# Kernel optimization log

Measured on AMD Instinct MI355X. Metric: run time of the kernel, lower is better.

Reference implementation:

```python
import jax, jax.numpy as jnp
import numpy as np

T, B, DG, DH, S = 24, 128, 256, 512, 3
LAM, ETA, EPS_A = 0.95, 0.5, 1e-6   # lambda_decay, eta, epsilon (A-update)
LN_EPS = 1e-5                        # torch LayerNorm default eps
EPS_N = 1e-6                         # norm clamp in inner loop


def setup_inputs() -> dict:
    key = jax.random.key(0)
    ks = jax.random.split(key, 3)
    return {
        "z_seq": jax.random.normal(ks[0], (T, B, DG), jnp.float32),
        "W_h": jax.random.normal(ks[1], (DH, DH), jnp.float32) * (2.0 / DH) ** 0.5,  # kaiming-ish
        "W_g": jax.random.normal(ks[2], (DH, DG), jnp.float32) * (1.0 / DG) ** 0.5,  # xavier-ish
        "b_h": jnp.zeros((DH,), jnp.float32),
        "gamma": jnp.ones((DH,), jnp.float32),
        "beta": jnp.zeros((DH,), jnp.float32),
        "alpha_fw": jnp.ones((1,), jnp.float32),
    }


def _layernorm(x, g, b):
    m = jnp.mean(x, -1, keepdims=True)
    v = jnp.mean((x - m) ** 2, -1, keepdims=True)
    return (x - m) * jax.lax.rsqrt(v + LN_EPS) * g + b


def _compute_k(a):
    k_pos = 1.0 + jax.nn.softplus(a)
    k_neg = 1.0 / (1.0 + jax.nn.softplus(-a))
    return jnp.where(a >= 0, k_pos, k_neg)


def reference(z_seq, W_h, W_g, b_h, gamma, beta, alpha_fw):
    k = _compute_k(alpha_fw[0])

    def step(carry, inp):
        h, A = carry            # h: [B, DH], A: [B, DH, DH]
        z_t, upd = inp          # z_t: [B, DG], upd: scalar bool (t < T-1)
        h_base = h @ W_h.T + z_t @ W_g.T + b_h
        h_s = jax.nn.relu(h_base)
        for _ in range(S):      # inner associative-memory iteration
            Ah = jnp.einsum('bij,bj->bi', A, h_s)
            dot = jnp.sum(h_s * Ah, -1, keepdims=True)
            n1 = jnp.maximum(jnp.linalg.norm(h_s, axis=-1, keepdims=True), EPS_N)
            n2 = jnp.maximum(jnp.linalg.norm(Ah, axis=-1, keepdims=True), EPS_N)
            R_pos = jnp.clip(dot / (n1 * n2), 0.0, 1.0)
            alpha_dyn = 1.0 - (1.0 - R_pos) ** k
            h_s = jax.nn.relu(_layernorm((1.0 - alpha_dyn ** 2) * h_base + alpha_dyn * Ah, gamma, beta))
        # fast-weight Hebbian update (skipped at the last timestep)
        hn2 = jnp.sum(h_s ** 2, -1, keepdims=True) + EPS_A            # [B, 1]
        delta = h_s[:, :, None] * h_s[:, None, :] / hn2[:, :, None]   # [B, DH, DH]
        A_new = jnp.where(upd, LAM * A + ETA * delta, A)
        return (h_s, A_new), None

    h0 = jnp.zeros((B, DH), z_seq.dtype)
    A0 = jnp.zeros((B, DH, DH), z_seq.dtype)
    upd = jnp.arange(T) < (T - 1)
    (h, A), _ = jax.lax.scan(step, (h0, A0), (z_seq, upd))
    return h
```

## Files before the change

kernel.cpp:

```cpp
#include <hip/hip_runtime.h>
#include <hip/hip_fp16.h>
#include <math.h>

#define T_STEPS 24
#define BATCH   128
#define DGI     256
#define DHI     512
#define S_ITERS 3
#define LAMBDA  0.95f
#define ETA     0.5f
#define EPS_A   1e-6f
#define LN_EPS  1e-5f
#define EPS_N   1e-6f
#define HIST_MAX 23

static __device__ __forceinline__ float dot2(unsigned int a, unsigned int b, float c) {
#if __has_builtin(__builtin_amdgcn_fdot2)
    typedef _Float16 h2v __attribute__((ext_vector_type(2)));
    return __builtin_amdgcn_fdot2(__builtin_bit_cast(h2v, a),
                                  __builtin_bit_cast(h2v, b), c, false);
#else
    const __half2 ha = __builtin_bit_cast(__half2, a);
    const __half2 hb = __builtin_bit_cast(__half2, b);
    const float2 fa = __half22float2(ha);
    const float2 fb = __half22float2(hb);
    return fmaf(fa.x, fb.x, fmaf(fa.y, fb.y, c));
#endif
}

__global__ __launch_bounds__(512)
void pack_wh_k(const float* __restrict__ Wh, unsigned int* __restrict__ P) {
    const int j2 = blockIdx.x;
    const int i  = threadIdx.x;
    const float2 w = *(const float2*)(Wh + (size_t)i * DHI + 2 * j2);
    const __half2 h = __floats2half2_rn(w.x, w.y);
    P[(size_t)j2 * DHI + i] = __builtin_bit_cast(unsigned int, h);
}

__global__ __launch_bounds__(512)
void zproj_k(const float* __restrict__ z_seq, const float* __restrict__ Wg,
             float* __restrict__ zp) {
    __shared__ __align__(16) float sh_z[8][DGI];
    const int b    = blockIdx.x;
    const int t0   = blockIdx.y * 8;
    const int tid  = threadIdx.x;
    const int lane = tid & 63;
    const int wave = tid >> 6;
    {
        const float4* src =
            (const float4*)(z_seq + ((size_t)(t0 + wave) * BATCH + b) * DGI);
        ((float4*)sh_z[wave])[lane] = src[lane];
    }
    __syncthreads();

    float acc[8];
    #pragma unroll
    for (int tt = 0; tt < 8; ++tt) acc[tt] = 0.f;
    const float4* wrow = (const float4*)(Wg + (size_t)tid * DGI);
    #pragma unroll 4
    for (int j4 = 0; j4 < DGI / 4; ++j4) {
        const float4 w = wrow[j4];
        #pragma unroll
        for (int tt = 0; tt < 8; ++tt) {
            const float4 z = ((const float4*)sh_z[tt])[j4];
            acc[tt] = fmaf(w.x, z.x, acc[tt]);
            acc[tt] = fmaf(w.y, z.y, acc[tt]);
            acc[tt] = fmaf(w.z, z.z, acc[tt]);
            acc[tt] = fmaf(w.w, z.w, acc[tt]);
        }
    }
    #pragma unroll
    for (int tt = 0; tt < 8; ++tt)
        zp[((size_t)b * T_STEPS + (t0 + tt)) * DHI + tid] = acc[tt];
}

__global__ __launch_bounds__(512)
void rnn_fp16w(const float* __restrict__ zp,
               const unsigned int* __restrict__ P,
               const float* __restrict__ b_h,
               const float* __restrict__ gamma,
               const float* __restrict__ beta,
               const float* __restrict__ alpha_fw,
               float* __restrict__ out) {
    __shared__ __align__(16) float  sh_hist[HIST_MAX][DHI];
    __shared__ __align__(16) float  sh_hs[2][DHI];
    __shared__ __align__(16) float  sh_G[HIST_MAX][64];
    __shared__ __align__(16) float4 sh_part[4][128];
    __shared__ __align__(16) unsigned int sh_h2[DHI / 2];
    __shared__ float  sh_coef[32];
    __shared__ float  sh_dot[32];
    __shared__ float2 sh_red[8];

    const int tid  = threadIdx.x;
    const int lane = tid & 63;
    const int wave = tid >> 6;
    const int b    = blockIdx.x;

    const float bh_r = b_h[tid];
    const float g_r  = gamma[tid];
    const float bt_r = beta[tid];

    float kpow;
    {
        const float a  = alpha_fw[0];
        const float ax = fabsf(a);
        const float sp = (ax > 20.f) ? ax : log1pf(expf(ax));
        kpow = (a >= 0.f) ? (1.f + sp) : (1.f / (1.f + sp));
    }

    for (int i = tid; i < HIST_MAX * 64; i += DHI) ((float*)sh_G)[i] = 0.f;
    __syncthreads();

    int   p = 0;
    float hs_i = 0.f, hbase_i = 0.f;

    for (int t = 0; t < T_STEPS; ++t) {
        const float zval = zp[((size_t)b * T_STEPS + t) * DHI + tid];
        if (t > 0) {
            const int i4 = tid & 127;
            const int jg = tid >> 7;
            const uint4* __restrict__ wp = (const uint4*)P;
            float4 acc = make_float4(0.f, 0.f, 0.f, 0.f);
            const int j2lo = jg * 64;
            #pragma unroll 8
            for (int jj = 0; jj < 64; ++jj) {
                const int j2 = j2lo + jj;
                const unsigned int hh = sh_h2[j2];
                const uint4 wv = wp[(size_t)j2 * 128 + i4];
                acc.x = dot2(wv.x, hh, acc.x);
                acc.y = dot2(wv.y, hh, acc.y);
                acc.z = dot2(wv.z, hh, acc.z);
                acc.w = dot2(wv.w, hh, acc.w);
            }
            sh_part[jg][i4] = acc;
            __syncthreads();
            const float* pp = (const float*)sh_part;
            hbase_i = bh_r + zval +
                      ((pp[tid] + pp[512 + tid]) + (pp[1024 + tid] + pp[1536 + tid]));
        } else {
            hbase_i = bh_r + zval;
        }
        hs_i = fmaxf(hbase_i, 0.f);
        p ^= 1;
        sh_hs[p][tid] = hs_i;
        __syncthreads();

        const int niter = (t == 0) ? 1 : S_ITERS;
        for (int it = 0; it < niter; ++it) {
            const float* hcur = sh_hs[p];
            float h8[8];
            #pragma unroll
            for (int q = 0; q < 8; ++q) h8[q] = hcur[lane + 64 * q];

            for (int s = wave; s <= t; s += 8) {
                float d = 0.f;
                if (s == t) {
                    #pragma unroll
                    for (int q = 0; q < 8; ++q) d = fmaf(h8[q], h8[q], d);
                } else {
                    const float* vr = sh_hist[s];
                    #pragma unroll
                    for (int q = 0; q < 8; ++q) d = fmaf(vr[lane + 64 * q], h8[q], d);
                }
                #pragma unroll
                for (int off = 32; off > 0; off >>= 1) d += __shfl_xor(d, off, 64);
                if (lane == 0) sh_dot[s] = d;
            }
            __syncthreads();

            float dl = 0.f, w_l = 0.f;
            if (lane < t) { dl = sh_dot[lane]; w_l = sh_coef[lane] * dl; }

            float gsum = 0.f, Ah = 0.f;
            for (int s = 0; s < t; ++s) {
                const float ws = sh_coef[s] * sh_dot[s];
                gsum = fmaf(ws, sh_G[s][lane], gsum);
                Ah   = fmaf(ws, sh_hist[s][tid], Ah);
            }
            float pa = w_l * dl;
            float pb = w_l * gsum;
            #pragma unroll
            for (int off = 32; off > 0; off >>= 1) {
                pa += __shfl_xor(pa, off, 64);
                pb += __shfl_xor(pb, off, 64);
            }
            const float n1 = fmaxf(sqrtf(sh_dot[t]), EPS_N);
            const float n2 = fmaxf(sqrtf(fmaxf(pb, 0.f)), EPS_N);
            float R = pa / (n1 * n2);
            R = fminf(fmaxf(R, 0.f), 1.f);
            const float alpha = 1.f - __powf(1.f - R, kpow);

            const float y = (1.f - alpha * alpha) * hbase_i + alpha * Ah;

            float q0 = y, q1 = y * y;
            #pragma unroll
            for (int off = 32; off > 0; off >>= 1) {
                q0 += __shfl_xor(q0, off, 64);
                q1 += __shfl_xor(q1, off, 64);
            }
            if (lane == 0) sh_red[wave] = make_float2(q0, q1);
            __syncthreads();

            float s0 = 0.f, s1 = 0.f;
            #pragma unroll
            for (int w = 0; w < 8; ++w) {
                const float2 r = sh_red[w];
                s0 += r.x; s1 += r.y;
            }
            const float mean = s0 * (1.f / DHI);
            const float var  = fmaf(s1, 1.f / DHI, -mean * mean);
            const float rstd = rsqrtf(var + LN_EPS);
            hs_i = fmaxf(fmaf((y - mean) * rstd, g_r, bt_r), 0.f);
            p ^= 1;
            sh_hs[p][tid] = hs_i;
            if (it == niter - 1 && t + 1 < T_STEPS) {
                const float partner = __shfl_xor(hs_i, 1);
                if (!(tid & 1)) {
                    const __half2 h2 = __floats2half2_rn(hs_i, partner);
                    sh_h2[tid >> 1] = __builtin_bit_cast(unsigned int, h2);
                }
            }
            __syncthreads();
        }

        if (t < T_STEPS - 1) {
            const float* hcur = sh_hs[p];
            float h8[8];
            #pragma unroll
            for (int q = 0; q < 8; ++q) h8[q] = hcur[lane + 64 * q];
            for (int s = wave; s <= t; s += 8) {
                float d = 0.f;
                if (s == t) {
                    #pragma unroll
                    for (int q = 0; q < 8; ++q) d = fmaf(h8[q], h8[q], d);
                } else {
                    const float* vr = sh_hist[s];
                    #pragma unroll
                    for (int q = 0; q < 8; ++q) d = fmaf(vr[lane + 64 * q], h8[q], d);
                }
                #pragma unroll
                for (int off = 32; off > 0; off >>= 1) d += __shfl_xor(d, off, 64);
                if (lane == 0) {
                    if (s == t) {
                        sh_G[t][t] = d;
                        sh_coef[t] = ETA / (d + EPS_A);
                    } else {
                        sh_G[t][s] = d;
                        sh_G[s][t] = d;
                    }
                }
            }
            if (tid < t) sh_coef[tid] *= LAMBDA;
            sh_hist[t][tid] = hs_i;
        } else {
            out[(size_t)b * DHI + tid] = hs_i;
        }
    }
}

__global__ __launch_bounds__(512)
void corernn_fb(const float* __restrict__ z_seq, const float* __restrict__ Wh,
                const float* __restrict__ Wg, const float* __restrict__ b_h,
                const float* __restrict__ gamma, const float* __restrict__ beta,
                const float* __restrict__ alpha_fw, float* __restrict__ out) {
    __shared__ __align__(16) float sh_hist[HIST_MAX][DHI];
    __shared__ __align__(16) float sh_hs[2][DHI];
    __shared__ __align__(16) float sh_G[HIST_MAX][64];
    __shared__ float  sh_coef[32];
    __shared__ float  sh_dot[32];
    __shared__ float2 sh_red[8];
    __shared__ __align__(16) float sh_z[DGI];

    const int tid  = threadIdx.x;
    const int lane = tid & 63;
    const int wave = tid >> 6;
    const int b    = blockIdx.x;
    const float bh_r = b_h[tid];
    const float g_r  = gamma[tid];
    const float bt_r = beta[tid];
    float kpow;
    {
        const float a  = alpha_fw[0];
        const float ax = fabsf(a);
        const float sp = (ax > 20.f) ? ax : log1pf(expf(ax));
        kpow = (a >= 0.f) ? (1.f + sp) : (1.f / (1.f + sp));
    }
    for (int i = tid; i < HIST_MAX * 64; i += DHI) ((float*)sh_G)[i] = 0.f;
    if (tid < DGI) sh_z[tid] = z_seq[(size_t)b * DGI + tid];
    __syncthreads();

    int p = 0;
    float hs_i = 0.f, hbase_i = 0.f;
    for (int t = 0; t < T_STEPS; ++t) {
        float a0 = bh_r, a1 = 0.f, a2 = 0.f, a3 = 0.f;
        {
            const float4* wrow = (const float4*)(Wg + (size_t)tid * DGI);
            const float4* z4   = (const float4*)sh_z;
            #pragma unroll 4
            for (int j4 = 0; j4 < DGI / 4; ++j4) {
                const float4 w = wrow[j4]; const float4 h = z4[j4];
                a0 = fmaf(w.x, h.x, a0); a1 = fmaf(w.y, h.y, a1);
                a2 = fmaf(w.z, h.z, a2); a3 = fmaf(w.w, h.w, a3);
            }
        }
        if (t > 0) {
            const float4* wrow = (const float4*)(Wh + (size_t)tid * DHI);
            const float4* h4   = (const float4*)sh_hs[p];
            #pragma unroll 4
            for (int j4 = 0; j4 < DHI / 4; ++j4) {
                const float4 w = wrow[j4]; const float4 h = h4[j4];
                a0 = fmaf(w.x, h.x, a0); a1 = fmaf(w.y, h.y, a1);
                a2 = fmaf(w.z, h.z, a2); a3 = fmaf(w.w, h.w, a3);
            }
        }
        hbase_i = (a0 + a1) + (a2 + a3);
        hs_i = fmaxf(hbase_i, 0.f);
        p ^= 1; sh_hs[p][tid] = hs_i;
        __syncthreads();

        const int niter = (t == 0) ? 1 : S_ITERS;
        for (int it = 0; it < niter; ++it) {
            const float* hcur = sh_hs[p];
            float h8[8];
            #pragma unroll
            for (int q = 0; q < 8; ++q) h8[q] = hcur[lane + 64 * q];
            for (int s = wave; s <= t; s += 8) {
                float d = 0.f;
                if (s == t) {
                    #pragma unroll
                    for (int q = 0; q < 8; ++q) d = fmaf(h8[q], h8[q], d);
                } else {
                    const float* vr = sh_hist[s];
                    #pragma unroll
                    for (int q = 0; q < 8; ++q) d = fmaf(vr[lane + 64 * q], h8[q], d);
                }
                #pragma unroll
                for (int off = 32; off > 0; off >>= 1) d += __shfl_xor(d, off, 64);
                if (lane == 0) sh_dot[s] = d;
            }
            __syncthreads();
            float dl = 0.f, w_l = 0.f;
            if (lane < t) { dl = sh_dot[lane]; w_l = sh_coef[lane] * dl; }
            float gsum = 0.f, Ah = 0.f;
            for (int s = 0; s < t; ++s) {
                const float ws = sh_coef[s] * sh_dot[s];
                gsum = fmaf(ws, sh_G[s][lane], gsum);
                Ah   = fmaf(ws, sh_hist[s][tid], Ah);
            }
            float pa = w_l * dl, pb = w_l * gsum;
            #pragma unroll
            for (int off = 32; off > 0; off >>= 1) {
                pa += __shfl_xor(pa, off, 64);
                pb += __shfl_xor(pb, off, 64);
            }
            const float n1 = fmaxf(sqrtf(sh_dot[t]), EPS_N);
            const float n2 = fmaxf(sqrtf(fmaxf(pb, 0.f)), EPS_N);
            float R = fminf(fmaxf(pa / (n1 * n2), 0.f), 1.f);
            const float alpha = 1.f - __powf(1.f - R, kpow);
            const float y = (1.f - alpha * alpha) * hbase_i + alpha * Ah;
            float q0 = y, q1 = y * y;
            #pragma unroll
            for (int off = 32; off > 0; off >>= 1) {
                q0 += __shfl_xor(q0, off, 64);
                q1 += __shfl_xor(q1, off, 64);
            }
            if (lane == 0) sh_red[wave] = make_float2(q0, q1);
            __syncthreads();
            float s0 = 0.f, s1 = 0.f;
            #pragma unroll
            for (int w = 0; w < 8; ++w) { const float2 r = sh_red[w]; s0 += r.x; s1 += r.y; }
            const float mean = s0 * (1.f / DHI);
            const float var  = fmaf(s1, 1.f / DHI, -mean * mean);
            const float rstd = rsqrtf(var + LN_EPS);
            hs_i = fmaxf(fmaf((y - mean) * rstd, g_r, bt_r), 0.f);
            p ^= 1; sh_hs[p][tid] = hs_i;
            if (it == niter - 1 && t + 1 < T_STEPS && tid < DGI)
                sh_z[tid] = z_seq[((size_t)(t + 1) * BATCH + b) * DGI + tid];
            __syncthreads();
        }

        if (t < T_STEPS - 1) {
            const float* hcur = sh_hs[p];
            float h8[8];
            #pragma unroll
            for (int q = 0; q < 8; ++q) h8[q] = hcur[lane + 64 * q];
            for (int s = wave; s <= t; s += 8) {
                float d = 0.f;
                if (s == t) {
                    #pragma unroll
                    for (int q = 0; q < 8; ++q) d = fmaf(h8[q], h8[q], d);
                } else {
                    const float* vr = sh_hist[s];
                    #pragma unroll
                    for (int q = 0; q < 8; ++q) d = fmaf(vr[lane + 64 * q], h8[q], d);
                }
                #pragma unroll
                for (int off = 32; off > 0; off >>= 1) d += __shfl_xor(d, off, 64);
                if (lane == 0) {
                    if (s == t) { sh_G[t][t] = d; sh_coef[t] = ETA / (d + EPS_A); }
                    else        { sh_G[t][s] = d; sh_G[s][t] = d; }
                }
            }
            if (tid < t) sh_coef[tid] *= LAMBDA;
            sh_hist[t][tid] = hs_i;
        } else {
            out[(size_t)b * DHI + tid] = hs_i;
        }
    }
}

extern "C" void kernel_launch(void* const* d_in, const int* in_sizes, int n_in,
                              void* d_out, int out_size, void* d_ws, size_t ws_size,
                              hipStream_t stream) {
    const float* z_seq    = (const float*)d_in[0];
    const float* W_h      = (const float*)d_in[1];
    const float* W_g      = (const float*)d_in[2];
    const float* b_h      = (const float*)d_in[3];
    const float* gamma    = (const float*)d_in[4];
    const float* beta     = (const float*)d_in[5];
    const float* alpha_fw = (const float*)d_in[6];
    float* out = (float*)d_out;

    const size_t zp_elems = (size_t)BATCH * T_STEPS * DHI;
    const size_t p_elems  = (size_t)(DHI / 2) * DHI;
    const size_t needed   = zp_elems * sizeof(float) + p_elems * sizeof(unsigned int);
    if (ws_size >= needed) {
        float* zp = (float*)d_ws;
        unsigned int* P = (unsigned int*)(zp + zp_elems);
        pack_wh_k<<<DHI / 2, DHI, 0, stream>>>(W_h, P);
        zproj_k<<<dim3(BATCH, T_STEPS / 8), 512, 0, stream>>>(z_seq, W_g, zp);
        rnn_fp16w<<<BATCH, DHI, 0, stream>>>(zp, P, b_h, gamma, beta, alpha_fw, out);
    } else {
        corernn_fb<<<BATCH, DHI, 0, stream>>>(z_seq, W_h, W_g, b_h, gamma, beta,
                                              alpha_fw, out);
    }
}
```

Before: 409.3 us.

## Compute LayerNorm stats algebraically and restructure history reductions and projections

The LayerNorm mean and variance inside the inner loop are now derived from precomputed scalar sums over the history (row sums, dots with h_base, the Gram-weighted norm), which removes a block-wide reduction and barrier per iteration. The history is also kept in a transposed float4 layout so each thread accumulates Ah and the Gram terms four steps at a time. Hidden-state halves are broadcast with readlane instead of LDS reads, and the next step's z projection is prefetched early. The z projection now uses a transposed W_g with readlane broadcasts, which needs an extra transpose kernel and more workspace. The algebraic variance can lose precision through cancellation, so it is clamped at zero.

```diff
diff --git a/kernel.cpp b/kernel.cpp
--- a/kernel.cpp
+++ b/kernel.cpp
@@ -13,6 +13,7 @@
 #define LN_EPS  1e-5f
 #define EPS_N   1e-6f
 #define HIST_MAX 23
+#define NG4      6
 
 static __device__ __forceinline__ float dot2(unsigned int a, unsigned int b, float c) {
 #if __has_builtin(__builtin_amdgcn_fdot2)
@@ -28,6 +29,49 @@
 #endif
 }
 
+static __device__ __forceinline__ unsigned int rdlane_u(unsigned int v, int l) {
+#if __has_builtin(__builtin_amdgcn_readlane)
+    return __builtin_amdgcn_readlane(v, l);
+#else
+    return __shfl((int)v, l, 64);
+#endif
+}
+static __device__ __forceinline__ float rdlane_f(float v, int l) {
+    return __uint_as_float(rdlane_u(__float_as_uint(v), l));
+}
+
+static __device__ __forceinline__ float wsum(float v) {
+    #pragma unroll
+    for (int off = 32; off > 0; off >>= 1) v += __shfl_xor(v, off, 64);
+    return v;
+}
+static __device__ __forceinline__ float dot8(float4 a, float4 b, float4 c, float4 d) {
+    float r = a.x * c.x;
+    r = fmaf(a.y, c.y, r); r = fmaf(a.z, c.z, r); r = fmaf(a.w, c.w, r);
+    r = fmaf(b.x, d.x, r); r = fmaf(b.y, d.y, r); r = fmaf(b.z, d.z, r);
+    r = fmaf(b.w, d.w, r);
+    return r;
+}
+static __device__ __forceinline__ float sum8(float4 a, float4 b) {
+    return ((a.x + a.y) + (a.z + a.w)) + ((b.x + b.y) + (b.z + b.w));
+}
+
+__global__ void transpose_k(const float* __restrict__ src, float* __restrict__ dst,
+                            int R, int C) {
+    __shared__ float tile[32][33];
+    const int tx = threadIdx.x & 31;
+    const int ty = threadIdx.x >> 5;
+    const int c0 = blockIdx.x * 32;
+    const int r0 = blockIdx.y * 32;
+    #pragma unroll
+    for (int i = 0; i < 32; i += 8)
+        tile[ty + i][tx] = src[(size_t)(r0 + ty + i) * C + (c0 + tx)];
+    __syncthreads();
+    #pragma unroll
+    for (int i = 0; i < 32; i += 8)
+        dst[(size_t)(c0 + ty + i) * R + (r0 + tx)] = tile[tx][ty + i];
+}
+
 __global__ __launch_bounds__(512)
 void pack_wh_k(const float* __restrict__ Wh, unsigned int* __restrict__ P) {
     const int j2 = blockIdx.x;
@@ -38,9 +82,10 @@
 }
 
 __global__ __launch_bounds__(512)
-void zproj_k(const float* __restrict__ z_seq, const float* __restrict__ Wg,
+void zproj_k(const float* __restrict__ z_seq, const float* __restrict__ WgT,
              float* __restrict__ zp) {
-    __shared__ __align__(16) float sh_z[8][DGI];
+    __shared__ __align__(16) float  sh_z[8][DGI];
+    __shared__ __align__(16) float4 sh_acc[8][4][128];
     const int b    = blockIdx.x;
     const int t0   = blockIdx.y * 8;
     const int tid  = threadIdx.x;
@@ -53,43 +98,64 @@
     }
     __syncthreads();
 
-    float acc[8];
-    #pragma unroll
-    for (int tt = 0; tt < 8; ++tt) acc[tt] = 0.f;
-    const float4* wrow = (const float4*)(Wg + (size_t)tid * DGI);
+    const int i4  = tid & 127;
+    const int jg  = tid >> 7;
+    const int jlo = jg * 64;
+    float zreg[8];
+    #pragma unroll
+    for (int tt = 0; tt < 8; ++tt) zreg[tt] = sh_z[tt][jlo + lane];
+
+    float4 acc[8];
+    #pragma unroll
+    for (int tt = 0; tt < 8; ++tt) acc[tt] = make_float4(0.f, 0.f, 0.f, 0.f);
+
+    const float4* w4 = (const float4*)WgT;
     #pragma unroll 4
-    for (int j4 = 0; j4 < DGI / 4; ++j4) {
-        const float4 w = wrow[j4];
+    for (int jj = 0; jj < 64; ++jj) {
+        const float4 wv = w4[(size_t)(jlo + jj) * 128 + i4];
         #pragma unroll
         for (int tt = 0; tt < 8; ++tt) {
-            const float4 z = ((const float4*)sh_z[tt])[j4];
-            acc[tt] = fmaf(w.x, z.x, acc[tt]);
-            acc[tt] = fmaf(w.y, z.y, acc[tt]);
-            acc[tt] = fmaf(w.z, z.z, acc[tt]);
-            acc[tt] = fmaf(w.w, z.w, acc[tt]);
-        }
-    }
-    #pragma unroll
-    for (int tt = 0; tt < 8; ++tt)
-        zp[((size_t)b * T_STEPS + (t0 + tt)) * DHI + tid] = acc[tt];
+            const float zv = rdlane_f(zreg[tt], jj);
+            acc[tt].x = fmaf(wv.x, zv, acc[tt].x);
+            acc[tt].y = fmaf(wv.y, zv, acc[tt].y);
+            acc[tt].z = fmaf(wv.z, zv, acc[tt].z);
+            acc[tt].w = fmaf(wv.w, zv, acc[tt].w);
+        }
+    }
+    #pragma unroll
+    for (int tt = 0; tt < 8; ++tt) sh_acc[tt][jg][i4] = acc[tt];
+    __syncthreads();
+
+    const float* af = (const float*)sh_acc;
+    #pragma unroll
+    for (int tt = 0; tt < 8; ++tt) {
+        const int o = tt * 4 * 512;
+        const float v = (af[o + tid] + af[o + 512 + tid]) +
+                        (af[o + 1024 + tid] + af[o + 1536 + tid]);
+        zp[((size_t)b * T_STEPS + t0 + tt) * DHI + tid] = v;
+    }
 }
 
 __global__ __launch_bounds__(512)
-void rnn_fp16w(const float* __restrict__ zp,
-               const unsigned int* __restrict__ P,
-               const float* __restrict__ b_h,
-               const float* __restrict__ gamma,
-               const float* __restrict__ beta,
-               const float* __restrict__ alpha_fw,
-               float* __restrict__ out) {
+void rnn_v3(const float* __restrict__ zp,
+            const unsigned int* __restrict__ P,
+            const float* __restrict__ b_h,
+            const float* __restrict__ gamma,
+            const float* __restrict__ beta,
+            const float* __restrict__ alpha_fw,
+            float* __restrict__ out) {
     __shared__ __align__(16) float  sh_hist[HIST_MAX][DHI];
+    __shared__ __align__(16) float4 sh_hT4[NG4][DHI];
+    __shared__ __align__(16) float4 sh_G4[NG4][64];
     __shared__ __align__(16) float  sh_hs[2][DHI];
-    __shared__ __align__(16) float  sh_G[HIST_MAX][64];
+    __shared__ __align__(16) float  sh_hb[DHI];
     __shared__ __align__(16) float4 sh_part[4][128];
     __shared__ __align__(16) unsigned int sh_h2[DHI / 2];
-    __shared__ float  sh_coef[32];
-    __shared__ float  sh_dot[32];
-    __shared__ float2 sh_red[8];
+    __shared__ __align__(16) float  sh_coef[32];
+    __shared__ __align__(16) float  sh_dot[32];
+    __shared__ __align__(16) float  sh_dhb[32];
+    __shared__ __align__(16) float  sh_rsum[32];
+    __shared__ float sh_misc[2];
 
     const int tid  = threadIdx.x;
     const int lane = tid & 63;
@@ -108,25 +174,33 @@
         kpow = (a >= 0.f) ? (1.f + sp) : (1.f / (1.f + sp));
     }
 
-    for (int i = tid; i < HIST_MAX * 64; i += DHI) ((float*)sh_G)[i] = 0.f;
+    {
+        const float4 z4 = make_float4(0.f, 0.f, 0.f, 0.f);
+        for (int i = tid; i < NG4 * DHI; i += DHI) ((float4*)sh_hT4)[i] = z4;
+        if (tid < NG4 * 64) ((float4*)sh_G4)[tid] = z4;
+        if (tid < 32) { sh_coef[tid] = 0.f; sh_dot[tid] = 0.f;
+                        sh_dhb[tid]  = 0.f; sh_rsum[tid] = 0.f; }
+        if (tid < 2) sh_misc[tid] = 0.f;
+    }
     __syncthreads();
 
     int   p = 0;
     float hs_i = 0.f, hbase_i = 0.f;
+    const size_t zbase = (size_t)b * T_STEPS * DHI + tid;
+    float zv = zp[zbase];
 
     for (int t = 0; t < T_STEPS; ++t) {
-        const float zval = zp[((size_t)b * T_STEPS + t) * DHI + tid];
         if (t > 0) {
             const int i4 = tid & 127;
             const int jg = tid >> 7;
             const uint4* __restrict__ wp = (const uint4*)P;
+            const unsigned int hreg = sh_h2[(jg << 6) | lane];
+            const int base = (jg << 6) * 128 + i4;
             float4 acc = make_float4(0.f, 0.f, 0.f, 0.f);
-            const int j2lo = jg * 64;
             #pragma unroll 8
             for (int jj = 0; jj < 64; ++jj) {
-                const int j2 = j2lo + jj;
-                const unsigned int hh = sh_h2[j2];
-                const uint4 wv = wp[(size_t)j2 * 128 + i4];
+                const unsigned int hh = rdlane_u(hreg, jj);
+                const uint4 wv = wp[base + jj * 128];
                 acc.x = dot2(wv.x, hh, acc.x);
                 acc.y = dot2(wv.y, hh, acc.y);
                 acc.z = dot2(wv.z, hh, acc.z);
@@ -135,81 +209,97 @@
             sh_part[jg][i4] = acc;
             __syncthreads();
             const float* pp = (const float*)sh_part;
-            hbase_i = bh_r + zval +
+            hbase_i = bh_r + zv +
                       ((pp[tid] + pp[512 + tid]) + (pp[1024 + tid] + pp[1536 + tid]));
         } else {
-            hbase_i = bh_r + zval;
-        }
+            hbase_i = bh_r + zv;
+        }
+        sh_hb[tid] = hbase_i;
         hs_i = fmaxf(hbase_i, 0.f);
         p ^= 1;
         sh_hs[p][tid] = hs_i;
         __syncthreads();
 
+        if (t + 1 < T_STEPS) zv = zp[zbase + (size_t)(t + 1) * DHI];
+
         const int niter = (t == 0) ? 1 : S_ITERS;
         for (int it = 0; it < niter; ++it) {
-            const float* hcur = sh_hs[p];
-            float h8[8];
-            #pragma unroll
-            for (int q = 0; q < 8; ++q) h8[q] = hcur[lane + 64 * q];
-
-            for (int s = wave; s <= t; s += 8) {
-                float d = 0.f;
-                if (s == t) {
-                    #pragma unroll
-                    for (int q = 0; q < 8; ++q) d = fmaf(h8[q], h8[q], d);
-                } else {
-                    const float* vr = sh_hist[s];
-                    #pragma unroll
-                    for (int q = 0; q < 8; ++q) d = fmaf(vr[lane + 64 * q], h8[q], d);
-                }
-                #pragma unroll
-                for (int off = 32; off > 0; off >>= 1) d += __shfl_xor(d, off, 64);
-                if (lane == 0) sh_dot[s] = d;
+            {
+                const float4* h4p = (const float4*)sh_hs[p];
+                const float4 ha = h4p[lane], hc = h4p[64 + lane];
+                float4 ba, bc;
+                if (it == 0) {
+                    const float4* b4p = (const float4*)sh_hb;
+                    ba = b4p[lane]; bc = b4p[64 + lane];
+                }
+                for (int s = wave; s <= t; s += 8) {
+                    if (s == t) {
+                        float d = dot8(ha, hc, ha, hc);
+                        if (it == 0) {
+                            float s1 = sum8(ba, bc);
+                            float s2 = dot8(ba, bc, ba, bc);
+                            d = wsum(d); s1 = wsum(s1); s2 = wsum(s2);
+                            if (lane == 0) { sh_dot[t] = d;
+                                             sh_misc[0] = s1; sh_misc[1] = s2; }
+                        } else {
+                            d = wsum(d);
+                            if (lane == 0) sh_dot[t] = d;
+                        }
+                    } else {
+                        const float4* v4 = (const float4*)sh_hist[s];
+                        const float4 va = v4[lane], vc = v4[64 + lane];
+                        float d = dot8(va, vc, ha, hc);
+                        if (it == 0) {
+                            float e = dot8(va, vc, ba, bc);
+                            d = wsum(d); e = wsum(e);
+                            if (lane == 0) { sh_dot[s] = d; sh_dhb[s] = e; }
+                        } else {
+                            d = wsum(d);
+                            if (lane == 0) sh_dot[s] = d;
+                        }
+                    }
+                }
             }
             __syncthreads();
 
-            float dl = 0.f, w_l = 0.f;
-            if (lane < t) { dl = sh_dot[lane]; w_l = sh_coef[lane] * dl; }
-
-            float gsum = 0.f, Ah = 0.f;
-            for (int s = 0; s < t; ++s) {
-                const float ws = sh_coef[s] * sh_dot[s];
-                gsum = fmaf(ws, sh_G[s][lane], gsum);
-                Ah   = fmaf(ws, sh_hist[s][tid], Ah);
-            }
-            float pa = w_l * dl;
-            float pb = w_l * gsum;
-            #pragma unroll
-            for (int off = 32; off > 0; off >>= 1) {
-                pa += __shfl_xor(pa, off, 64);
-                pb += __shfl_xor(pb, off, 64);
-            }
+            float pa = 0.f, SA = 0.f, SHA = 0.f, gsum = 0.f, Ah = 0.f;
+            {
+                const float4* c4 = (const float4*)sh_coef;
+                const float4* d4 = (const float4*)sh_dot;
+                const float4* e4 = (const float4*)sh_dhb;
+                const float4* r4 = (const float4*)sh_rsum;
+                const int ng = (t + 4) >> 2;
+                for (int g = 0; g < ng; ++g) {
+                    const float4 cc = c4[g], dd = d4[g], ee = e4[g], rr = r4[g];
+                    const float4 gg = sh_G4[g][lane];
+                    const float4 hv = sh_hT4[g][tid];
+                    const float w0 = cc.x * dd.x, w1 = cc.y * dd.y;
+                    const float w2 = cc.z * dd.z, w3 = cc.w * dd.w;
+                    pa   = fmaf(w0, dd.x, fmaf(w1, dd.y, fmaf(w2, dd.z, fmaf(w3, dd.w, pa))));
+                    SA   = fmaf(w0, rr.x, fmaf(w1, rr.y, fmaf(w2, rr.z, fmaf(w3, rr.w, SA))));
+                    SHA  = fmaf(w0, ee.x, fmaf(w1, ee.y, fmaf(w2, ee.z, fmaf(w3, ee.w, SHA))));
+                    gsum = fmaf(w0, gg.x, fmaf(w1, gg.y, fmaf(w2, gg.z, fmaf(w3, gg.w, gsum))));
+                    Ah   = fmaf(w0, hv.x, fmaf(w1, hv.y, fmaf(w2, hv.z, fmaf(w3, hv.w, Ah))));
+                }
+            }
+            const float wl = (lane < 32) ? sh_coef[lane] * sh_dot[lane] : 0.f;
+            const float pb = wsum(wl * gsum);
+
             const float n1 = fmaxf(sqrtf(sh_dot[t]), EPS_N);
             const float n2 = fmaxf(sqrtf(fmaxf(pb, 0.f)), EPS_N);
             float R = pa / (n1 * n2);
             R = fminf(fmaxf(R, 0.f), 1.f);
             const float alpha = 1.f - __powf(1.f - R, kpow);
-
-            const float y = (1.f - alpha * alpha) * hbase_i + alpha * Ah;
-
-            float q0 = y, q1 = y * y;
-            #pragma unroll
-            for (int off = 32; off > 0; off >>= 1) {
-                q0 += __shfl_xor(q0, off, 64);
-                q1 += __shfl_xor(q1, off, 64);
-            }
-            if (lane == 0) sh_red[wave] = make_float2(q0, q1);
-            __syncthreads();
-
-            float s0 = 0.f, s1 = 0.f;
-            #pragma unroll
-            for (int w = 0; w < 8; ++w) {
-                const float2 r = sh_red[w];
-                s0 += r.x; s1 += r.y;
-            }
-            const float mean = s0 * (1.f / DHI);
-            const float var  = fmaf(s1, 1.f / DHI, -mean * mean);
+            const float c = 1.f - alpha * alpha;
+
+            const float S1 = sh_misc[0], S2 = sh_misc[1];
+            const float mean = (c * S1 + alpha * SA) * (1.f / DHI);
+            float var = (c * c * S2 + 2.f * c * alpha * SHA + alpha * alpha * pb)
+                        * (1.f / DHI) - mean * mean;
+            var = fmaxf(var, 0.f);
             const float rstd = rsqrtf(var + LN_EPS);
+
+            const float y = fmaf(c, hbase_i, alpha * Ah);
             hs_i = fmaxf(fmaf((y - mean) * rstd, g_r, bt_r), 0.f);
             p ^= 1;
             sh_hs[p][tid] = hs_i;
@@ -224,34 +314,32 @@
         }
 
         if (t < T_STEPS - 1) {
-            const float* hcur = sh_hs[p];
-            float h8[8];
-            #pragma unroll
-            for (int q = 0; q < 8; ++q) h8[q] = hcur[lane + 64 * q];
+            const float4* h4p = (const float4*)sh_hs[p];
+            const float4 ha = h4p[lane], hc = h4p[64 + lane];
             for (int s = wave; s <= t; s += 8) {
-                float d = 0.f;
                 if (s == t) {
-                    #pragma unroll
-                    for (int q = 0; q < 8; ++q) d = fmaf(h8[q], h8[q], d);
+                    float d  = dot8(ha, hc, ha, hc);
+                    float rs = sum8(ha, hc);
+                    d = wsum(d); rs = wsum(rs);
+                    if (lane == 0) {
+                        ((float*)&sh_G4[t >> 2][t])[t & 3] = d;
+                        sh_coef[t] = ETA / (d + EPS_A);
+                        sh_rsum[t] = rs;
+                    }
                 } else {
-                    const float* vr = sh_hist[s];
-                    #pragma unroll
-                    for (int q = 0; q < 8; ++q) d = fmaf(vr[lane + 64 * q], h8[q], d);
-                }
-                #pragma unroll
-                for (int off = 32; off > 0; off >>= 1) d += __shfl_xor(d, off, 64);
-                if (lane == 0) {
-                    if (s == t) {
-                        sh_G[t][t] = d;
-                        sh_coef[t] = ETA / (d + EPS_A);
-                    } else {
-                        sh_G[t][s] = d;
-                        sh_G[s][t] = d;
+                    const float4* v4 = (const float4*)sh_hist[s];
+                    const float4 va = v4[lane], vc = v4[64 + lane];
+                    float d = dot8(va, vc, ha, hc);
+                    d = wsum(d);
+                    if (lane == 0) {
+                        ((float*)&sh_G4[t >> 2][s])[t & 3] = d;
+                        ((float*)&sh_G4[s >> 2][t])[s & 3] = d;
                     }
                 }
             }
             if (tid < t) sh_coef[tid] *= LAMBDA;
             sh_hist[t][tid] = hs_i;
+            ((float*)&sh_hT4[t >> 2][tid])[t & 3] = hs_i;
         } else {
             out[(size_t)b * DHI + tid] = hs_i;
         }
@@ -421,15 +509,19 @@
     const float* alpha_fw = (const float*)d_in[6];
     float* out = (float*)d_out;
 
-    const size_t zp_elems = (size_t)BATCH * T_STEPS * DHI;
-    const size_t p_elems  = (size_t)(DHI / 2) * DHI;
-    const size_t needed   = zp_elems * sizeof(float) + p_elems * sizeof(unsigned int);
+    const size_t zp_elems  = (size_t)BATCH * T_STEPS * DHI;
+    const size_t wgt_elems = (size_t)DGI * DHI;
+    const size_t p_elems   = (size_t)(DHI / 2) * DHI;
+    const size_t needed = (zp_elems + wgt_elems) * sizeof(float)
+                        + p_elems * sizeof(unsigned int);
     if (ws_size >= needed) {
-        float* zp = (float*)d_ws;
-        unsigned int* P = (unsigned int*)(zp + zp_elems);
+        float* zp  = (float*)d_ws;
+        float* WgT = zp + zp_elems;
+        unsigned int* P = (unsigned int*)(WgT + wgt_elems);
+        transpose_k<<<dim3(DGI / 32, DHI / 32), 256, 0, stream>>>(W_g, WgT, DHI, DGI);
         pack_wh_k<<<DHI / 2, DHI, 0, stream>>>(W_h, P);
-        zproj_k<<<dim3(BATCH, T_STEPS / 8), 512, 0, stream>>>(z_seq, W_g, zp);
-        rnn_fp16w<<<BATCH, DHI, 0, stream>>>(zp, P, b_h, gamma, beta, alpha_fw, out);
+        zproj_k<<<dim3(BATCH, T_STEPS / 8), 512, 0, stream>>>(z_seq, WgT, zp);
+        rnn_v3<<<BATCH, DHI, 0, stream>>>(zp, P, b_h, gamma, beta, alpha_fw, out);
     } else {
         corernn_fb<<<BATCH, DHI, 0, stream>>>(z_seq, W_h, W_g, b_h, gamma, beta,
                                               alpha_fw, out);
```

Result: faster. 366.3 us (-10.5%).
